# Kernel tuning notes

Measured on AMD Instinct MI355X. Metric: run time of the kernel, lower is better.

The kernel has to match this reference:

```python
import jax, jax.numpy as jnp
import numpy as np

N, E, D, ETYPES = 20000, 200000, 256, 16

def _gelu(x):
    return jax.nn.gelu(x, approximate=False)

def setup_inputs() -> dict:
    key = jax.random.key(0)
    ks = jax.random.split(key, 24)
    s = lambda k, shape, fan: (jax.random.normal(k, shape, jnp.float32) / np.sqrt(fan)).astype(jnp.float32)
    inp = {}
    inp['node_embeddings'] = jax.random.normal(ks[0], (N, D), jnp.float32)
    inp['edge_index'] = jax.random.randint(ks[1], (2, E), 0, N, jnp.int64 if jax.config.jax_enable_x64 else jnp.int32)
    inp['edge_type'] = jax.random.randint(ks[2], (E,), 0, ETYPES, jnp.int32)
    inp['task_embedding'] = jax.random.normal(ks[3], (D,), jnp.float32)
    inp['edge_emb'] = s(ks[4], (ETYPES, D), D)
    inp['msg_W'] = s(ks[5], (D, D), D); inp['msg_b'] = jnp.zeros((D,), jnp.float32)
    inp['att_W1'] = s(ks[6], (4 * D, D), 4 * D); inp['att_b1'] = jnp.zeros((D,), jnp.float32)
    inp['att_W2'] = s(ks[7], (D, 1), D); inp['att_b2'] = jnp.zeros((1,), jnp.float32)
    inp['edge_scale'] = jnp.asarray(0.5, jnp.float32)
    inp['ma_W1'] = s(ks[8], (D, 2 * D), D); inp['ma_b1'] = jnp.zeros((2 * D,), jnp.float32)
    inp['ma_W2'] = s(ks[9], (2 * D, 2 * D), 2 * D); inp['ma_b2'] = jnp.zeros((2 * D,), jnp.float32)
    inp['up_W1'] = s(ks[10], (2 * D, D), 2 * D); inp['up_b1'] = jnp.zeros((D,), jnp.float32)
    inp['up_W2'] = s(ks[11], (D, D), D); inp['up_b2'] = jnp.zeros((D,), jnp.float32)
    inp['ua_W1'] = s(ks[12], (D, 2 * D), D); inp['ua_b1'] = jnp.zeros((2 * D,), jnp.float32)
    inp['ua_W2'] = s(ks[13], (2 * D, 2 * D), 2 * D); inp['ua_b2'] = jnp.zeros((2 * D,), jnp.float32)
    inp['ln_g'] = jnp.ones((D,), jnp.float32); inp['ln_b'] = jnp.zeros((D,), jnp.float32)
    return inp

def reference(node_embeddings, edge_index, edge_type, task_embedding, edge_emb,
              msg_W, msg_b, att_W1, att_b1, att_W2, att_b2, edge_scale,
              ma_W1, ma_b1, ma_W2, ma_b2, up_W1, up_b1, up_W2, up_b2,
              ua_W1, ua_b1, ua_W2, ua_b2, ln_g, ln_b):
    n_nodes = node_embeddings.shape[0]
    src, dst = edge_index[0], edge_index[1]
    e = edge_emb[edge_type]                       # [E, D]
    x_src = node_embeddings[src]                  # [E, D]
    x_dst = node_embeddings[dst]                  # [E, D]
    messages = (x_src + e) @ msg_W + msg_b        # [E, D]
    # edge attention over [x_src, x_dst, edge_repr, task]
    task_rep = jnp.broadcast_to(task_embedding, (src.shape[0], task_embedding.shape[0]))
    att_in = jnp.concatenate([x_src, x_dst, e, task_rep], axis=-1)  # [E, 4D]
    edge_delta = jnp.tanh(_gelu(att_in @ att_W1 + att_b1) @ att_W2 + att_b2)  # [E, 1]
    edge_weight = 1.0 + edge_scale * edge_delta   # [E, 1]
    # FiLM-style message adapter from task embedding
    ma = _gelu(task_embedding @ ma_W1 + ma_b1) @ ma_W2 + ma_b2      # [2D]
    msg_gamma, msg_beta = ma[:ma.shape[0] // 2], ma[ma.shape[0] // 2:]
    messages = messages * (1.0 + 0.5 * jnp.tanh(msg_gamma)) + msg_beta
    messages = messages * edge_weight
    # scatter-add aggregation with degree normalization
    agg = jax.ops.segment_sum(messages, dst, num_segments=n_nodes)            # [N, D]
    deg = jax.ops.segment_sum(edge_weight[:, 0], dst, num_segments=n_nodes)   # [N]
    agg = agg / jnp.maximum(deg, 1.0)[:, None]
    ua = _gelu(task_embedding @ ua_W1 + ua_b1) @ ua_W2 + ua_b2      # [2D]
    upd_gamma, upd_beta = ua[:ua.shape[0] // 2], ua[ua.shape[0] // 2:]
    agg = agg * (1.0 + 0.5 * jnp.tanh(upd_gamma)) + upd_beta
    upd_in = jnp.concatenate([node_embeddings, agg], axis=-1)       # [N, 2D]
    updated = _gelu(upd_in @ up_W1 + up_b1) @ up_W2 + up_b2         # [N, D]
    y = node_embeddings + updated
    mu = jnp.mean(y, axis=-1, keepdims=True)
    var = jnp.mean((y - mu) ** 2, axis=-1, keepdims=True)
    return (y - mu) / jnp.sqrt(var + 1e-5) * ln_g + ln_b
```

## Files before the change

### kernel.cpp

```cpp
#include <hip/hip_runtime.h>
#include <hip/hip_bf16.h>

#define NN 20000
#define NE 200000

typedef __bf16 bf16x8 __attribute__((ext_vector_type(8)));
typedef float f32x4 __attribute__((ext_vector_type(4)));
typedef unsigned short u16x8 __attribute__((ext_vector_type(8)));

constexpr int TAB_MSG_SCALE = 0;
constexpr int TAB_MSG_BETA  = 256;
constexpr int TAB_UPD_SCALE = 512;
constexpr int TAB_UPD_BETA  = 768;
constexpr int TAB_TASKC     = 1024;
constexpr int TAB_ECM       = 1280;
constexpr size_t OFF_WPRET = 40960;
constexpr size_t OFF_W1T   = 434176;
constexpr size_t OFF_W2T   = 696320;
constexpr size_t OFF_CNT   = 827392;
constexpr size_t OFF_PTRS  = 907392;
constexpr size_t OFF_PWORK = 987648;
constexpr size_t OFF_SRCET = 1067648;
constexpr size_t OFF_UPDB  = 1867648;
constexpr size_t OFF_G     = 12107648;
constexpr size_t OFF_P2B   = 32587648;
constexpr size_t WS_NEED   = 42827648;

constexpr int GEMM_BLOCKS = (NN + 63)/64;

__device__ __forceinline__ float bf2f(unsigned short u){
  union { unsigned int i; float f; } v; v.i = ((unsigned int)u) << 16; return v.f;
}
__device__ __forceinline__ unsigned short f2bf(float f){
  __bf16 h = (__bf16)f; unsigned short u; __builtin_memcpy(&u, &h, 2); return u;
}
__device__ __forceinline__ float gelu_f(float x){
  return 0.5f * x * (1.0f + erff(x * 0.70710678118654752f));
}
__device__ __forceinline__ float gelu_fast(float x){
  return x / (1.0f + __expf(-1.702f * x));
}
__device__ __forceinline__ float tanh_fast(float x){
  float e = __expf(2.0f * x);
  return 1.0f - 2.0f / (e + 1.0f);
}
__device__ __forceinline__ float sum16(const float* p){
  float a = ((p[0]+p[1])+(p[2]+p[3])) + ((p[4]+p[5])+(p[6]+p[7]));
  float b = ((p[8]+p[9])+(p[10]+p[11])) + ((p[12]+p[13])+(p[14]+p[15]));
  return a + b;
}

__global__ __launch_bounds__(256) void k_setup(
    const float* __restrict__ task, const float* __restrict__ eemb,
    const float* __restrict__ msg_W, const float* __restrict__ msg_b,
    const float* __restrict__ att_W1, const float* __restrict__ att_b1,
    const float* __restrict__ ma_W1, const float* __restrict__ ma_b1,
    const float* __restrict__ ma_W2, const float* __restrict__ ma_b2,
    const float* __restrict__ ua_W1, const float* __restrict__ ua_b1,
    const float* __restrict__ ua_W2, const float* __restrict__ ua_b2,
    const float* __restrict__ up_W1, const float* __restrict__ up_W2,
    const int* __restrict__ eidx,
    float* __restrict__ tabs,
    unsigned short* __restrict__ WpreT, unsigned short* __restrict__ W1T,
    unsigned short* __restrict__ W2T, int* __restrict__ cnt)
{
  __shared__ float s_in[512];
  __shared__ float s_h[512];
  int bb = blockIdx.x, tid = threadIdx.x;
  if (bb >= 1315){
    int e = (bb - 1315)*256 + tid;
    if (e < NE) atomicAdd(&cnt[eidx[NE + e]], 1);
    return;
  }
  if (bb >= 35){
    int b = bb - 35;
    if (b < 768){
      int n = b;
      float v;
      if (n < 256)      v = msg_W[tid*256 + n];
      else if (n < 512) v = att_W1[tid*256 + (n - 256)];
      else              v = att_W1[(256 + tid)*256 + (n - 512)];
      WpreT[n*256 + tid] = f2bf(v);
    } else if (b < 1024){
      int n = b - 768;
      W1T[n*512 + tid]       = f2bf(up_W1[tid*256 + n]);
      W1T[n*512 + 256 + tid] = f2bf(up_W1[(256 + tid)*256 + n]);
    } else {
      int n = b - 1024;
      W2T[n*256 + tid] = f2bf(up_W2[tid*256 + n]);
    }
    return;
  }
  int b = bb;
  if (b < 2){
    const float* W1 = b ? ua_W1 : ma_W1;  const float* b1 = b ? ua_b1 : ma_b1;
    const float* W2 = b ? ua_W2 : ma_W2;  const float* b2 = b ? ua_b2 : ma_b2;
    s_in[tid] = task[tid];
    __syncthreads();
    #pragma unroll
    for (int jj = 0; jj < 2; ++jj){
      int j = tid + jj*256;
      float pacc[16];
      #pragma unroll
      for (int u = 0; u < 16; ++u) pacc[u] = 0.f;
      for (int k0 = 0; k0 < 256; k0 += 16){
        float wv[16];
        #pragma unroll
        for (int u = 0; u < 16; ++u) wv[u] = W1[(k0 + u)*512 + j];
        #pragma unroll
        for (int u = 0; u < 16; ++u) pacc[u] += s_in[k0 + u] * wv[u];
      }
      s_h[j] = gelu_f(b1[j] + sum16(pacc));
    }
    __syncthreads();
    float o[2];
    #pragma unroll
    for (int jj = 0; jj < 2; ++jj){
      int j = tid + jj*256;
      float pacc[16];
      #pragma unroll
      for (int u = 0; u < 16; ++u) pacc[u] = 0.f;
      for (int k0 = 0; k0 < 512; k0 += 16){
        float wv[16];
        #pragma unroll
        for (int u = 0; u < 16; ++u) wv[u] = W2[(k0 + u)*512 + j];
        #pragma unroll
        for (int u = 0; u < 16; ++u) pacc[u] += s_h[k0 + u] * wv[u];
      }
      o[jj] = b2[j] + sum16(pacc);
    }
    float* scale = tabs + (b ? TAB_UPD_SCALE : TAB_MSG_SCALE);
    float* beta  = tabs + (b ? TAB_UPD_BETA  : TAB_MSG_BETA);
    scale[tid] = 1.0f + 0.5f * tanhf(o[0]);
    beta[tid]  = o[1];
  } else if (b == 2){
    s_in[tid] = task[tid];
    __syncthreads();
    float pacc[16];
    #pragma unroll
    for (int u = 0; u < 16; ++u) pacc[u] = 0.f;
    for (int k0 = 0; k0 < 256; k0 += 16){
      float wv[16];
      #pragma unroll
      for (int u = 0; u < 16; ++u) wv[u] = att_W1[(768 + k0 + u)*256 + tid];
      #pragma unroll
      for (int u = 0; u < 16; ++u) pacc[u] += s_in[k0 + u] * wv[u];
    }
    tabs[TAB_TASKC + tid] = att_b1[tid] + sum16(pacc);
  } else if (b < 19){
    int t = b - 3;
    s_in[tid] = eemb[t*256 + tid];
    __syncthreads();
    float pacc[16];
    #pragma unroll
    for (int u = 0; u < 16; ++u) pacc[u] = 0.f;
    for (int k0 = 0; k0 < 256; k0 += 16){
      float wv[16];
      #pragma unroll
      for (int u = 0; u < 16; ++u) wv[u] = msg_W[(k0 + u)*256 + tid];
      #pragma unroll
      for (int u = 0; u < 16; ++u) pacc[u] += s_in[k0 + u] * wv[u];
    }
    tabs[TAB_ECM + t*512 + ((tid >> 2) << 3) + 4 + (tid & 3)] = msg_b[tid] + sum16(pacc);
  } else {
    int t = b - 19;
    s_in[tid] = eemb[t*256 + tid];
    __syncthreads();
    float pacc[16];
    #pragma unroll
    for (int u = 0; u < 16; ++u) pacc[u] = 0.f;
    for (int k0 = 0; k0 < 256; k0 += 16){
      float wv[16];
      #pragma unroll
      for (int u = 0; u < 16; ++u) wv[u] = att_W1[(512 + k0 + u)*256 + tid];
      #pragma unroll
      for (int u = 0; u < 16; ++u) pacc[u] += s_in[k0 + u] * wv[u];
    }
    tabs[TAB_ECM + t*512 + ((tid >> 2) << 3) + (tid & 3)] = sum16(pacc);
  }
}

__global__ __launch_bounds__(256) void k_gemm_pre(
    const float* __restrict__ X, const unsigned short* __restrict__ WpreT,
    const float* __restrict__ tabs,
    unsigned short* __restrict__ G, unsigned short* __restrict__ P2b,
    const int* __restrict__ cnt, int* __restrict__ ptrs, int* __restrict__ pwork)
{
  __shared__ __align__(16) unsigned short s_b[16*256];
  int tid = threadIdx.x;
  if (blockIdx.x == GEMM_BLOCKS){
    int* s = (int*)s_b;
    constexpr int PER = (NN + 255)/256;
    int i0 = tid*PER;
    int tot = 0;
    for (int j = 0; j < PER; ++j){
      int i = i0 + j;
      if (i < NN) tot += cnt[i];
    }
    s[tid] = tot;
    __syncthreads();
    #pragma unroll
    for (int off = 1; off < 256; off <<= 1){
      int t = (tid >= off) ? s[tid - off] : 0;
      __syncthreads();
      s[tid] += t;
      __syncthreads();
    }
    int run = s[tid] - tot;
    for (int j = 0; j < PER; ++j){
      int i = i0 + j;
      if (i < NN){
        ptrs[i]  = run;
        pwork[i] = run;
        run += cnt[i];
      }
    }
    if (tid == 255) ptrs[NN] = s[255];
    return;
  }
  int wv = tid >> 6, lane = tid & 63;
  int m0 = blockIdx.x*64 + wv*16;
  bool valid = (m0 < NN);
  int lo = lane & 15, hi = lane >> 4;
  bf16x8 a[8];
  if (valid){
    const float* xrow = X + (size_t)(m0 + lo)*256 + hi*8;
    #pragma unroll
    for (int kc = 0; kc < 8; ++kc){
      float4 f0 = *(const float4*)(xrow + kc*32);
      float4 f1 = *(const float4*)(xrow + kc*32 + 4);
      bf16x8 v;
      v[0]=(__bf16)f0.x; v[1]=(__bf16)f0.y; v[2]=(__bf16)f0.z; v[3]=(__bf16)f0.w;
      v[4]=(__bf16)f1.x; v[5]=(__bf16)f1.y; v[6]=(__bf16)f1.z; v[7]=(__bf16)f1.w;
      a[kc] = v;
    }
  }
  int sn = tid >> 4, sk0 = (tid & 15)*16;
  int sswz = (sn & 7) << 3;
  int rswz = (lo & 7) << 3;
  for (int nt = 0; nt < 48; ++nt){
    __syncthreads();
    {
      const unsigned short* gsrc = WpreT + (size_t)(nt*16 + sn)*256 + sk0;
      uint4 d0 = *(const uint4*)(gsrc);
      uint4 d1 = *(const uint4*)(gsrc + 8);
      *(uint4*)(s_b + sn*256 + (sk0 ^ sswz))       = d0;
      *(uint4*)(s_b + sn*256 + ((sk0 + 8) ^ sswz)) = d1;
    }
    __syncthreads();
    if (!valid) continue;
    f32x4 acc = {0.f, 0.f, 0.f, 0.f};
    #pragma unroll
    for (int kc = 0; kc < 8; ++kc){
      bf16x8 bfrag = *(const bf16x8*)(s_b + lo*256 + ((kc*32 + hi*8) ^ rswz));
      acc = __builtin_amdgcn_mfma_f32_16x16x32_bf16(a[kc], bfrag, acc, 0, 0, 0);
    }
    int n0 = nt*16;
    if (nt < 16){
      int j = n0 + lo;
      int elem = ((j >> 2) << 3) + 4 + (j & 3);
      unsigned short* grow = G + (size_t)(m0 + hi*4)*512 + elem;
      #pragma unroll
      for (int r = 0; r < 4; ++r) grow[(size_t)r*512] = f2bf(acc[r]);
    } else if (nt < 32){
      int j = n0 - 256 + lo;
      int elem = ((j >> 2) << 3) + (j & 3);
      unsigned short* grow = G + (size_t)(m0 + hi*4)*512 + elem;
      #pragma unroll
      for (int r = 0; r < 4; ++r) grow[(size_t)r*512] = f2bf(acc[r]);
    } else {
      int j = n0 - 512 + lo;
      float tcadd = tabs[TAB_TASKC + j];
      unsigned short* prow = P2b + (size_t)(m0 + hi*4)*256 + j;
      #pragma unroll
      for (int r = 0; r < 4; ++r) prow[(size_t)r*256] = f2bf(acc[r] + tcadd);
    }
  }
}

__global__ __launch_bounds__(256) void k_csr_build(
    const int* __restrict__ eidx, const int* __restrict__ etype,
    int* __restrict__ pwork, unsigned int* __restrict__ srcet)
{
  int e = blockIdx.x*256 + threadIdx.x;
  if (e < NE){
    int dst = eidx[NE + e];
    int pos = atomicAdd(&pwork[dst], 1);
    srcet[pos] = (unsigned int)eidx[e] | ((unsigned int)etype[e] << 16);
  }
}

__global__ __launch_bounds__(256) void k_agg(
    const int* __restrict__ ptrs, const unsigned int* __restrict__ srcet,
    const unsigned short* __restrict__ G, const unsigned short* __restrict__ P2b,
    const float* __restrict__ tabs, const float* __restrict__ attW2,
    const float* __restrict__ attb2, const float* __restrict__ escale,
    unsigned short* __restrict__ updB)
{
  int node = blockIdx.x*4 + (threadIdx.x >> 6);
  if (node >= NN) return;
  int lane = threadIdx.x & 63, c0 = lane*4;
  ushort4 p2 = *(const ushort4*)(P2b + (size_t)node*256 + c0);
  float q0 = bf2f(p2.x), q1 = bf2f(p2.y), q2 = bf2f(p2.z), q3 = bf2f(p2.w);
  float4 w2 = *(const float4*)(attW2 + c0);
  float sc = escale[0], bb = attb2[0];
  float4 ms = *(const float4*)(tabs + TAB_MSG_SCALE + c0);
  float4 mb = *(const float4*)(tabs + TAB_MSG_BETA  + c0);
  float4 us = *(const float4*)(tabs + TAB_UPD_SCALE + c0);
  float4 ub = *(const float4*)(tabs + TAB_UPD_BETA  + c0);
  const float* ecm_base = tabs + TAB_ECM + (lane << 3);
  int start = ptrs[node], end = ptrs[node + 1];
  float ax = 0.f, ay = 0.f, az = 0.f, aw = 0.f, W = 0.f;
  unsigned int se0 = 0, se1 = 0;
  u16x8 g0 = {0,0,0,0,0,0,0,0};
  if (start < end){
    se0 = srcet[start];
    g0 = *(const u16x8*)(G + (size_t)(se0 & 0xFFFFu)*512 + lane*8);
    if (start + 1 < end) se1 = srcet[start + 1];
  }
  for (int i = start; i < end; ++i){
    u16x8 g1 = g0;
    unsigned int se2 = 0;
    if (i + 1 < end) g1 = *(const u16x8*)(G + (size_t)(se1 & 0xFFFFu)*512 + lane*8);
    if (i + 2 < end) se2 = srcet[i + 2];
    int et = (int)(se0 >> 16);
    const float* ecm = ecm_base + et*512;
    float4 ec = *(const float4*)(ecm);
    float4 em = *(const float4*)(ecm + 4);
    float part = gelu_fast(bf2f(g0[0]) + q0 + ec.x)*w2.x
               + gelu_fast(bf2f(g0[1]) + q1 + ec.y)*w2.y
               + gelu_fast(bf2f(g0[2]) + q2 + ec.z)*w2.z
               + gelu_fast(bf2f(g0[3]) + q3 + ec.w)*w2.w;
    #pragma unroll
    for (int off = 32; off; off >>= 1) part += __shfl_xor(part, off);
    float w = 1.0f + sc*tanh_fast(part + bb);
    ax += w*(bf2f(g0[4]) + em.x);
    ay += w*(bf2f(g0[5]) + em.y);
    az += w*(bf2f(g0[6]) + em.z);
    aw += w*(bf2f(g0[7]) + em.w);
    W += w;
    se0 = se1; se1 = se2; g0 = g1;
  }
  float d = fmaxf(W, 1.0f), rd = 1.0f / d;
  ushort4 st = { f2bf((ms.x*ax + mb.x*W)*rd*us.x + ub.x),
                 f2bf((ms.y*ay + mb.y*W)*rd*us.y + ub.y),
                 f2bf((ms.z*az + mb.z*W)*rd*us.z + ub.z),
                 f2bf((ms.w*aw + mb.w*W)*rd*us.w + ub.w) };
  *(ushort4*)(updB + (size_t)node*256 + c0) = st;
}

__device__ __forceinline__ bf16x8 ldA(const float* xrow, const unsigned short* urow, int ke){
  if (ke < 256){
    float4 f0 = *(const float4*)(xrow + ke);
    float4 f1 = *(const float4*)(xrow + ke + 4);
    bf16x8 v;
    v[0]=(__bf16)f0.x; v[1]=(__bf16)f0.y; v[2]=(__bf16)f0.z; v[3]=(__bf16)f0.w;
    v[4]=(__bf16)f1.x; v[5]=(__bf16)f1.y; v[6]=(__bf16)f1.z; v[7]=(__bf16)f1.w;
    return v;
  }
  return *(const bf16x8*)(urow + (ke - 256));
}

__global__ __launch_bounds__(256) void k_mlp(
    const float* __restrict__ X, const unsigned short* __restrict__ updB,
    const unsigned short* __restrict__ W1T, const unsigned short* __restrict__ W2T,
    const float* __restrict__ up_b1, const float* __restrict__ up_b2,
    const float* __restrict__ ln_g, const float* __restrict__ ln_b,
    float* __restrict__ out)
{
  __shared__ __align__(16) unsigned short s_H[32*256];
  __shared__ float s_sum[4*32], s_sq[4*32];
  __shared__ float s_mu[32], s_rs[32];
  int m0 = blockIdx.x*32;
  int tid = threadIdx.x;
  int wv = tid >> 6, lane = tid & 63, lo = lane & 15, hi = lane >> 4;

  const float* x0 = X + (size_t)(m0 + lo)*256;
  const float* x1 = x0 + 16*256;
  const unsigned short* u0 = updB + (size_t)(m0 + lo)*256;
  const unsigned short* u1 = u0 + 16*256;

  f32x4 acc0[4], acc1[4];
  #pragma unroll
  for (int t = 0; t < 4; ++t){
    float b = up_b1[wv*64 + t*16 + lo];
    acc0[t] = (f32x4){b, b, b, b};
    acc1[t] = acc0[t];
  }
  #pragma unroll
  for (int kc = 0; kc < 16; ++kc){
    int ke = kc*32 + hi*8;
    bf16x8 a0 = ldA(x0, u0, ke);
    bf16x8 a1 = ldA(x1, u1, ke);
    #pragma unroll
    for (int t = 0; t < 4; ++t){
      int n = wv*64 + t*16 + lo;
      bf16x8 bf = *(const bf16x8*)(W1T + (size_t)n*512 + ke);
      acc0[t] = __builtin_amdgcn_mfma_f32_16x16x32_bf16(a0, bf, acc0[t], 0, 0, 0);
      acc1[t] = __builtin_amdgcn_mfma_f32_16x16x32_bf16(a1, bf, acc1[t], 0, 0, 0);
    }
  }
  #pragma unroll
  for (int t = 0; t < 4; ++t){
    #pragma unroll
    for (int r = 0; r < 4; ++r){
      int row0 = hi*4 + r, n = wv*64 + t*16 + lo;
      s_H[(row0 << 8) | (n ^ ((row0 & 7) << 3))] = f2bf(gelu_fast(acc0[t][r]));
      int row1 = row0 + 16;
      s_H[(row1 << 8) | (n ^ ((row1 & 7) << 3))] = f2bf(gelu_fast(acc1[t][r]));
    }
  }
  __syncthreads();

  f32x4 y0[4], y1[4];
  #pragma unroll
  for (int t = 0; t < 4; ++t){
    float b = up_b2[wv*64 + t*16 + lo];
    y0[t] = (f32x4){b, b, b, b};
    y1[t] = y0[t];
  }
  #pragma unroll
  for (int kc = 0; kc < 8; ++kc){
    int ke = kc*32 + hi*8;
    bf16x8 af0 = *(const bf16x8*)(s_H + ((lo << 8) | (ke ^ ((lo & 7) << 3))));
    int r1 = lo + 16;
    bf16x8 af1 = *(const bf16x8*)(s_H + ((r1 << 8) | (ke ^ ((r1 & 7) << 3))));
    #pragma unroll
    for (int t = 0; t < 4; ++t){
      int n = wv*64 + t*16 + lo;
      bf16x8 bf = *(const bf16x8*)(W2T + (size_t)n*256 + ke);
      y0[t] = __builtin_amdgcn_mfma_f32_16x16x32_bf16(af0, bf, y0[t], 0, 0, 0);
      y1[t] = __builtin_amdgcn_mfma_f32_16x16x32_bf16(af1, bf, y1[t], 0, 0, 0);
    }
  }

  #pragma unroll
  for (int t = 0; t < 4; ++t){
    #pragma unroll
    for (int r = 0; r < 4; ++r){
      int row0 = hi*4 + r, n = wv*64 + t*16 + lo;
      y0[t][r] += X[(size_t)(m0 + row0)*256 + n];
      y1[t][r] += X[(size_t)(m0 + row0 + 16)*256 + n];
    }
  }

  float ps[2][4], pq[2][4];
  #pragma unroll
  for (int r = 0; r < 4; ++r){
    float s0 = 0.f, q0 = 0.f, s1 = 0.f, q1 = 0.f;
    #pragma unroll
    for (int t = 0; t < 4; ++t){
      s0 += y0[t][r]; q0 += y0[t][r]*y0[t][r];
      s1 += y1[t][r]; q1 += y1[t][r]*y1[t][r];
    }
    #pragma unroll
    for (int off = 1; off < 16; off <<= 1){
      s0 += __shfl_xor(s0, off); q0 += __shfl_xor(q0, off);
      s1 += __shfl_xor(s1, off); q1 += __shfl_xor(q1, off);
    }
    ps[0][r] = s0; pq[0][r] = q0;
    ps[1][r] = s1; pq[1][r] = q1;
  }
  if (lo == 0){
    #pragma unroll
    for (int m = 0; m < 2; ++m){
      #pragma unroll
      for (int r = 0; r < 4; ++r){
        int row = m*16 + hi*4 + r;
        s_sum[wv*32 + row] = ps[m][r];
        s_sq [wv*32 + row] = pq[m][r];
      }
    }
  }
  __syncthreads();
  if (tid < 32){
    float sum = s_sum[tid] + s_sum[32 + tid] + s_sum[64 + tid] + s_sum[96 + tid];
    float sq  = s_sq[tid]  + s_sq[32 + tid]  + s_sq[64 + tid]  + s_sq[96 + tid];
    float mu = sum * (1.0f/256.0f);
    float var = sq * (1.0f/256.0f) - mu*mu;
    s_mu[tid] = mu;
    s_rs[tid] = rsqrtf(var + 1e-5f);
  }
  __syncthreads();

  #pragma unroll
  for (int t = 0; t < 4; ++t){
    int n = wv*64 + t*16 + lo;
    float lg = ln_g[n], lb = ln_b[n];
    #pragma unroll
    for (int r = 0; r < 4; ++r){
      int row0 = hi*4 + r, row1 = row0 + 16;
      out[(size_t)(m0 + row0)*256 + n] = (y0[t][r] - s_mu[row0]) * s_rs[row0] * lg + lb;
      out[(size_t)(m0 + row1)*256 + n] = (y1[t][r] - s_mu[row1]) * s_rs[row1] * lg + lb;
    }
  }
}

extern "C" void kernel_launch(void* const* d_in, const int* in_sizes, int n_in,
                              void* d_out, int out_size, void* d_ws, size_t ws_size,
                              hipStream_t stream)
{
  (void)in_sizes; (void)n_in; (void)out_size;
  if (ws_size < WS_NEED) return;
  const float* X      = (const float*)d_in[0];
  const int*   eidx   = (const int*)d_in[1];
  const int*   etype  = (const int*)d_in[2];
  const float* task   = (const float*)d_in[3];
  const float* eemb   = (const float*)d_in[4];
  const float* msg_W  = (const float*)d_in[5];
  const float* msg_b  = (const float*)d_in[6];
  const float* att_W1 = (const float*)d_in[7];
  const float* att_b1 = (const float*)d_in[8];
  const float* att_W2 = (const float*)d_in[9];
  const float* att_b2 = (const float*)d_in[10];
  const float* escale = (const float*)d_in[11];
  const float* ma_W1  = (const float*)d_in[12];
  const float* ma_b1  = (const float*)d_in[13];
  const float* ma_W2  = (const float*)d_in[14];
  const float* ma_b2  = (const float*)d_in[15];
  const float* up_W1  = (const float*)d_in[16];
  const float* up_b1  = (const float*)d_in[17];
  const float* up_W2  = (const float*)d_in[18];
  const float* up_b2  = (const float*)d_in[19];
  const float* ua_W1  = (const float*)d_in[20];
  const float* ua_b1  = (const float*)d_in[21];
  const float* ua_W2  = (const float*)d_in[22];
  const float* ua_b2  = (const float*)d_in[23];
  const float* ln_g   = (const float*)d_in[24];
  const float* ln_b   = (const float*)d_in[25];
  char* ws = (char*)d_ws;
  float* tabs = (float*)ws;
  unsigned short* WpreT = (unsigned short*)(ws + OFF_WPRET);
  unsigned short* W1T   = (unsigned short*)(ws + OFF_W1T);
  unsigned short* W2T   = (unsigned short*)(ws + OFF_W2T);
  int*          cnt   = (int*)(ws + OFF_CNT);
  int*          ptrs  = (int*)(ws + OFF_PTRS);
  int*          pwork = (int*)(ws + OFF_PWORK);
  unsigned int* srcet = (unsigned int*)(ws + OFF_SRCET);
  unsigned short* updB = (unsigned short*)(ws + OFF_UPDB);
  unsigned short* G    = (unsigned short*)(ws + OFF_G);
  unsigned short* P2b  = (unsigned short*)(ws + OFF_P2B);
  float* out = (float*)d_out;

  hipMemsetAsync(cnt, 0, (size_t)NN*4, stream);
  k_setup<<<2097, 256, 0, stream>>>(task, eemb, msg_W, msg_b, att_W1, att_b1,
                                    ma_W1, ma_b1, ma_W2, ma_b2,
                                    ua_W1, ua_b1, ua_W2, ua_b2,
                                    up_W1, up_W2, eidx,
                                    tabs, WpreT, W1T, W2T, cnt);
  k_gemm_pre<<<GEMM_BLOCKS + 1, 256, 0, stream>>>(X, WpreT, tabs, G, P2b,
                                                  cnt, ptrs, pwork);
  k_csr_build<<<(NE + 255)/256, 256, 0, stream>>>(eidx, etype, pwork, srcet);
  k_agg<<<(NN + 3)/4, 256, 0, stream>>>(ptrs, srcet, G, P2b, tabs,
                                        att_W2, att_b2, escale, updB);
  k_mlp<<<NN/32, 256, 0, stream>>>(X, updB, W1T, W2T, up_b1, up_b2,
                                   ln_g, ln_b, out);
}
```

Baseline: 242.0 us.

## Restructure pre-GEMM: 32-row blocks, waves split N tiles, B read from global

The pre-projection GEMM now gives each block 32 rows instead of 64. Each wave holds both 16-row A fragments and computes 12 of the 48 output column tiles, instead of every wave covering all 48 tiles for its own 16 rows. B fragments are loaded straight from global memory (expected to hit cache), which removes the LDS staging and the two barriers per tile. The trade-offs are that each block re-reads the A rows and that B reuse now depends on L1/L2, and the new mapping assumes NN is divisible by 32.

```diff
diff --git a/kernel.cpp b/kernel.cpp
--- a/kernel.cpp
+++ b/kernel.cpp
@@ -26,7 +26,7 @@
 constexpr size_t OFF_P2B   = 32587648;
 constexpr size_t WS_NEED   = 42827648;
 
-constexpr int GEMM_BLOCKS = (NN + 63)/64;
+constexpr int GEMM_BLOCKS = NN/32;
 
 __device__ __forceinline__ float bf2f(unsigned short u){
   union { unsigned int i; float f; } v; v.i = ((unsigned int)u) << 16; return v.f;
@@ -186,10 +186,9 @@
     unsigned short* __restrict__ G, unsigned short* __restrict__ P2b,
     const int* __restrict__ cnt, int* __restrict__ ptrs, int* __restrict__ pwork)
 {
-  __shared__ __align__(16) unsigned short s_b[16*256];
+  __shared__ int s_scan[256];
   int tid = threadIdx.x;
   if (blockIdx.x == GEMM_BLOCKS){
-    int* s = (int*)s_b;
     constexpr int PER = (NN + 255)/256;
     int i0 = tid*PER;
     int tot = 0;
@@ -197,16 +196,16 @@
       int i = i0 + j;
       if (i < NN) tot += cnt[i];
     }
-    s[tid] = tot;
+    s_scan[tid] = tot;
     __syncthreads();
     #pragma unroll
     for (int off = 1; off < 256; off <<= 1){
-      int t = (tid >= off) ? s[tid - off] : 0;
+      int t = (tid >= off) ? s_scan[tid - off] : 0;
       __syncthreads();
-      s[tid] += t;
+      s_scan[tid] += t;
       __syncthreads();
     }
-    int run = s[tid] - tot;
+    int run = s_scan[tid] - tot;
     for (int j = 0; j < PER; ++j){
       int i = i0 + j;
       if (i < NN){
@@ -215,65 +214,72 @@
         run += cnt[i];
       }
     }
-    if (tid == 255) ptrs[NN] = s[255];
+    if (tid == 255) ptrs[NN] = s_scan[255];
     return;
   }
   int wv = tid >> 6, lane = tid & 63;
-  int m0 = blockIdx.x*64 + wv*16;
-  bool valid = (m0 < NN);
+  int m0 = blockIdx.x*32;
   int lo = lane & 15, hi = lane >> 4;
-  bf16x8 a[8];
-  if (valid){
-    const float* xrow = X + (size_t)(m0 + lo)*256 + hi*8;
+  bf16x8 a0[8], a1[8];
+  {
+    const float* x0 = X + (size_t)(m0 + lo)*256 + hi*8;
+    const float* x1 = x0 + 16*256;
     #pragma unroll
     for (int kc = 0; kc < 8; ++kc){
-      float4 f0 = *(const float4*)(xrow + kc*32);
-      float4 f1 = *(const float4*)(xrow + kc*32 + 4);
+      float4 f0 = *(const float4*)(x0 + kc*32);
+      float4 f1 = *(const float4*)(x0 + kc*32 + 4);
       bf16x8 v;
       v[0]=(__bf16)f0.x; v[1]=(__bf16)f0.y; v[2]=(__bf16)f0.z; v[3]=(__bf16)f0.w;
       v[4]=(__bf16)f1.x; v[5]=(__bf16)f1.y; v[6]=(__bf16)f1.z; v[7]=(__bf16)f1.w;
-      a[kc] = v;
-    }
-  }
-  int sn = tid >> 4, sk0 = (tid & 15)*16;
-  int sswz = (sn & 7) << 3;
-  int rswz = (lo & 7) << 3;
-  for (int nt = 0; nt < 48; ++nt){
-    __syncthreads();
-    {
-      const unsigned short* gsrc = WpreT + (size_t)(nt*16 + sn)*256 + sk0;
-      uint4 d0 = *(const uint4*)(gsrc);
-      uint4 d1 = *(const uint4*)(gsrc + 8);
-      *(uint4*)(s_b + sn*256 + (sk0 ^ sswz))       = d0;
-      *(uint4*)(s_b + sn*256 + ((sk0 + 8) ^ sswz)) = d1;
-    }
-    __syncthreads();
-    if (!valid) continue;
-    f32x4 acc = {0.f, 0.f, 0.f, 0.f};
+      a0[kc] = v;
+      float4 g0 = *(const float4*)(x1 + kc*32);
+      float4 g1 = *(const float4*)(x1 + kc*32 + 4);
+      bf16x8 u;
+      u[0]=(__bf16)g0.x; u[1]=(__bf16)g0.y; u[2]=(__bf16)g0.z; u[3]=(__bf16)g0.w;
+      u[4]=(__bf16)g1.x; u[5]=(__bf16)g1.y; u[6]=(__bf16)g1.z; u[7]=(__bf16)g1.w;
+      a1[kc] = u;
+    }
+  }
+  const unsigned short* bbase = WpreT + (size_t)lo*256 + hi*8;
+  for (int t = 0; t < 12; ++t){
+    int nt = wv*12 + t;
+    const unsigned short* bcol = bbase + (size_t)nt*16*256;
+    f32x4 acc0 = {0.f, 0.f, 0.f, 0.f};
+    f32x4 acc1 = {0.f, 0.f, 0.f, 0.f};
     #pragma unroll
     for (int kc = 0; kc < 8; ++kc){
-      bf16x8 bfrag = *(const bf16x8*)(s_b + lo*256 + ((kc*32 + hi*8) ^ rswz));
-      acc = __builtin_amdgcn_mfma_f32_16x16x32_bf16(a[kc], bfrag, acc, 0, 0, 0);
+      bf16x8 bfrag = *(const bf16x8*)(bcol + kc*32);
+      acc0 = __builtin_amdgcn_mfma_f32_16x16x32_bf16(a0[kc], bfrag, acc0, 0, 0, 0);
+      acc1 = __builtin_amdgcn_mfma_f32_16x16x32_bf16(a1[kc], bfrag, acc1, 0, 0, 0);
     }
     int n0 = nt*16;
     if (nt < 16){
       int j = n0 + lo;
       int elem = ((j >> 2) << 3) + 4 + (j & 3);
-      unsigned short* grow = G + (size_t)(m0 + hi*4)*512 + elem;
-      #pragma unroll
-      for (int r = 0; r < 4; ++r) grow[(size_t)r*512] = f2bf(acc[r]);
+      unsigned short* g0p = G + (size_t)(m0 + hi*4)*512 + elem;
+      #pragma unroll
+      for (int r = 0; r < 4; ++r){
+        g0p[(size_t)r*512]        = f2bf(acc0[r]);
+        g0p[(size_t)(r + 16)*512] = f2bf(acc1[r]);
+      }
     } else if (nt < 32){
       int j = n0 - 256 + lo;
       int elem = ((j >> 2) << 3) + (j & 3);
-      unsigned short* grow = G + (size_t)(m0 + hi*4)*512 + elem;
-      #pragma unroll
-      for (int r = 0; r < 4; ++r) grow[(size_t)r*512] = f2bf(acc[r]);
+      unsigned short* g0p = G + (size_t)(m0 + hi*4)*512 + elem;
+      #pragma unroll
+      for (int r = 0; r < 4; ++r){
+        g0p[(size_t)r*512]        = f2bf(acc0[r]);
+        g0p[(size_t)(r + 16)*512] = f2bf(acc1[r]);
+      }
     } else {
       int j = n0 - 512 + lo;
       float tcadd = tabs[TAB_TASKC + j];
-      unsigned short* prow = P2b + (size_t)(m0 + hi*4)*256 + j;
-      #pragma unroll
-      for (int r = 0; r < 4; ++r) prow[(size_t)r*256] = f2bf(acc[r] + tcadd);
+      unsigned short* p0 = P2b + (size_t)(m0 + hi*4)*256 + j;
+      #pragma unroll
+      for (int r = 0; r < 4; ++r){
+        p0[(size_t)r*256]        = f2bf(acc0[r] + tcadd);
+        p0[(size_t)(r + 16)*256] = f2bf(acc1[r] + tcadd);
+      }
     }
   }
 }
```

Result: slower. 257.0 us (+6.2%).
